# Kernel optimization log

Hardware: AMD Instinct MI355X
Metric: run time of the kernel (lower is better)

## Reference

```python
import jax, jax.numpy as jnp
import numpy as np

NUM_BLOCKS = 8
SPARSITY = 0.01
HARD_FRAC = 1.0
HSF = 1  # hidden_size_factor
SCALE = 0.02


def _softshrink(v, lambd):
    return jnp.where(v > lambd, v - lambd, jnp.where(v < -lambd, v + lambd, jnp.zeros_like(v)))


def setup_inputs() -> dict:
    key = jax.random.key(0)
    ks = jax.random.split(key, 5)
    B, H, W, C = 8, 128, 128, 768
    bs = C // NUM_BLOCKS  # 96
    x = jax.random.normal(ks[0], (B, H, W, C), dtype=jnp.float32)
    w1 = SCALE * jax.random.normal(ks[1], (2, NUM_BLOCKS, bs, bs * HSF), dtype=jnp.float32)
    b1 = SCALE * jax.random.normal(ks[2], (2, NUM_BLOCKS, bs * HSF), dtype=jnp.float32)
    w2 = SCALE * jax.random.normal(ks[3], (2, NUM_BLOCKS, bs * HSF, bs), dtype=jnp.float32)
    b2 = SCALE * jax.random.normal(ks[4], (2, NUM_BLOCKS, bs), dtype=jnp.float32)
    return {"x": x, "w1": w1, "b1": b1, "w2": w2, "b2": b2}


def reference(x, w1, b1, w2, b2):
    B, H, W, C = x.shape
    bs = C // NUM_BLOCKS
    bias = x
    xf = jnp.fft.rfft2(x, axes=(1, 2), norm="ortho")  # [B,H,W//2+1,C] complex
    Wf = W // 2 + 1
    xf = xf.reshape(B, H, Wf, NUM_BLOCKS, bs)
    total_modes = H // 2 + 1
    kept = int(total_modes * HARD_FRAC)
    h0 = total_modes - kept
    h1 = min(total_modes + kept, H)  # python slicing clips; mirror that statically
    w1k = min(kept, Wf)
    xs = xf[:, h0:h1, :w1k]  # kept-modes window
    xr, xi = jnp.real(xs), jnp.imag(xs)
    # block-diagonal complex MLP layer 1 with relu
    o1r = jax.nn.relu(jnp.einsum("bhwni,nio->bhwno", xr, w1[0]) - jnp.einsum("bhwni,nio->bhwno", xi, w1[1]) + b1[0])
    o1i = jax.nn.relu(jnp.einsum("bhwni,nio->bhwno", xi, w1[0]) + jnp.einsum("bhwni,nio->bhwno", xr, w1[1]) + b1[1])
    # layer 2
    o2r = jnp.einsum("bhwno,noi->bhwni", o1r, w2[0]) - jnp.einsum("bhwno,noi->bhwni", o1i, w2[1]) + b2[0]
    o2i = jnp.einsum("bhwno,noi->bhwni", o1i, w2[0]) + jnp.einsum("bhwno,noi->bhwni", o1r, w2[1]) + b2[1]
    # softshrink applied to real and imag components separately (torch stacks then shrinks)
    o2r = _softshrink(o2r, SPARSITY)
    o2i = _softshrink(o2i, SPARSITY)
    out = jnp.zeros((B, H, Wf, NUM_BLOCKS, bs), dtype=xf.dtype)
    out = out.at[:, h0:h1, :w1k].set(o2r + 1j * o2i)
    out = out.reshape(B, H, Wf, C)
    y = jnp.fft.irfft2(out, s=(H, W), axes=(1, 2), norm="ortho")
    return y + bias
```

## Files before the change

### kernel.cpp

```cpp
#include <hip/hip_runtime.h>


#define B_DIM 8
#define H_DIM 128
#define W_DIM 128
#define C_DIM 768
#define WF    65
#define NBLK  8
#define BS    96
#define LAMBDA 0.01f
#define TWO_PI_OVER_N 0.04908738521234052f

__device__ __forceinline__ int brev7(int v) { return (int)(__brev((unsigned)v) >> 25); }

__global__ __launch_bounds__(256) void k1_rfft_w(const float* __restrict__ x,
                                                 float2* __restrict__ S) {
    const int blk   = blockIdx.x;
    const int ctile = blk % 24;
    const int bh    = blk / 24;
    const int c0    = ctile * 32;

    __shared__ float2 zs[W_DIM][17];
    __shared__ float cs[64], sn[64];

    const int tid = threadIdx.x;
    if (tid < 64) {
        float sv, cv;
        sincosf(TWO_PI_OVER_N * (float)tid, &sv, &cv);
        cs[tid] = cv; sn[tid] = sv;
    }
    const float2* xp = (const float2*)(x + (size_t)bh * (W_DIM * C_DIM) + c0);
    for (int idx = tid; idx < W_DIM * 16; idx += 256) {
        int w = idx >> 4, u = idx & 15;
        zs[w][u] = xp[(size_t)w * (C_DIM / 2) + u];
    }
    __syncthreads();

    const int u  = tid & 15;
    const int j0 = tid >> 4;
    #pragma unroll
    for (int s = 0; s < 7; ++s) {
        const int ls = 6 - s;
        const int m  = 1 << ls;
        #pragma unroll
        for (int jj = 0; jj < 4; ++jj) {
            const int j  = j0 + jj * 16;
            const int t  = j & (m - 1);
            const int i0 = 2 * j - t;
            const int i1 = i0 + m;
            const int tw = t << (6 - ls);
            float2 a = zs[i0][u], b = zs[i1][u];
            const float cv = cs[tw], sv = sn[tw];
            float dx = a.x - b.x, dy = a.y - b.y;
            zs[i0][u] = make_float2(a.x + b.x, a.y + b.y);
            zs[i1][u] = make_float2(fmaf(dx, cv,  dy * sv),
                                    fmaf(dy, cv, -dx * sv));
        }
        __syncthreads();
    }

    for (int pos = tid; pos < WF * 16; pos += 256) {
        int kw = pos >> 4, uu = pos & 15;
        float2 Za = zs[brev7(kw)][uu];
        float2 Zb = zs[brev7((128 - kw) & 127)][uu];
        const float sc = 0.5f * 0.0078125f;
        float xcx = (Za.x + Zb.x) * sc;
        float xcy = (Za.y - Zb.y) * sc;
        float xdx = (Za.y + Zb.y) * sc;
        float xdy = (Zb.x - Za.x) * sc;
        float4* Srow = (float4*)(S + ((size_t)bh * WF + kw) * C_DIM + c0);
        Srow[uu] = make_float4(xcx, xcy, xdx, xdy);
    }
}

template <bool INV>
__global__ __launch_bounds__(256) void k_fft_h(float2* __restrict__ S) {
    const int blk   = blockIdx.x;
    const int ctile = blk % 24;
    const int rest  = blk / 24;
    const int kw    = rest % WF;
    const int b     = rest / WF;
    const int c0    = ctile * 32;

    __shared__ float2 zs[H_DIM][33];
    __shared__ float cs[64], sn[64];

    const int tid = threadIdx.x;
    if (tid < 64) {
        float sv, cv;
        sincosf(TWO_PI_OVER_N * (float)tid, &sv, &cv);
        cs[tid] = cv; sn[tid] = sv;
    }
    const size_t base = (((size_t)b * H_DIM) * WF + kw) * C_DIM + c0;
    const size_t hstr = (size_t)WF * C_DIM;
    for (int idx = tid; idx < H_DIM * 32; idx += 256) {
        int h = idx >> 5, c = idx & 31;
        zs[h][c] = S[base + (size_t)h * hstr + c];
    }
    __syncthreads();

    const int c  = tid & 31;
    const int j0 = tid >> 5;
    #pragma unroll
    for (int s = 0; s < 7; ++s) {
        const int ls = INV ? s : (6 - s);
        const int m  = 1 << ls;
        #pragma unroll
        for (int jj = 0; jj < 8; ++jj) {
            const int j  = j0 + jj * 8;
            const int t  = j & (m - 1);
            const int i0 = 2 * j - t;
            const int i1 = i0 + m;
            const int tw = t << (6 - ls);
            float2 a  = zs[i0][c];
            float2 bv = zs[i1][c];
            const float cv = cs[tw], sv = sn[tw];
            if (!INV) {
                float dx = a.x - bv.x, dy = a.y - bv.y;
                zs[i0][c] = make_float2(a.x + bv.x, a.y + bv.y);
                zs[i1][c] = make_float2(fmaf(dx, cv,  dy * sv),
                                        fmaf(dy, cv, -dx * sv));
            } else {
                float btx = fmaf(bv.x, cv, -bv.y * sv);
                float bty = fmaf(bv.y, cv,  bv.x * sv);
                zs[i0][c] = make_float2(a.x + btx, a.y + bty);
                zs[i1][c] = make_float2(a.x - btx, a.y - bty);
            }
        }
        __syncthreads();
    }

    for (int idx = tid; idx < H_DIM * 32; idx += 256) {
        int h = idx >> 5, cc = idx & 31;
        float2 v = zs[h][cc];
        if (INV) { v.x *= 0.0078125f; v.y *= 0.0078125f; }
        S[base + (size_t)h * hstr + cc] = v;
    }
}

__device__ __forceinline__ float softshrinkf(float v) {
    return v > LAMBDA ? v - LAMBDA : (v < -LAMBDA ? v + LAMBDA : 0.f);
}

__global__ __launch_bounds__(256) void k3_mlp(float2* __restrict__ S,
                                              const float* __restrict__ w1,
                                              const float* __restrict__ b1,
                                              const float* __restrict__ w2,
                                              const float* __restrict__ b2) {
    const int n     = blockIdx.y;
    const int pbase = blockIdx.x * 32;
    const int c0    = n * BS;

    __shared__ float2 xin[32][BS];
    __shared__ float2 o1s[32][BS];

    const int tid = threadIdx.x;
    for (int idx = tid; idx < 32 * BS; idx += 256) {
        int p = idx / BS, c = idx - p * BS;
        xin[p][c] = S[(size_t)(pbase + p) * C_DIM + c0 + c];
    }
    __syncthreads();

    const int oq = tid & 31;
    const int pq = tid >> 5;

    float ar[3][4], ai[3][4];
    #pragma unroll
    for (int k = 0; k < 3; ++k)
        #pragma unroll
        for (int jj = 0; jj < 4; ++jj) { ar[k][jj] = 0.f; ai[k][jj] = 0.f; }

    const float* W1r = w1 + (size_t)n * BS * BS + oq;
    const float* W1i = w1 + (size_t)(NBLK + n) * BS * BS + oq;
    for (int i = 0; i < BS; ++i) {
        float2 z0 = xin[pq][i];
        float2 z1 = xin[pq + 8][i];
        float2 z2 = xin[pq + 16][i];
        float2 z3 = xin[pq + 24][i];
        #pragma unroll
        for (int k = 0; k < 3; ++k) {
            float wr = W1r[i * BS + 32 * k];
            float wi = W1i[i * BS + 32 * k];
            ar[k][0] = fmaf(z0.x, wr, fmaf(-z0.y, wi, ar[k][0]));
            ai[k][0] = fmaf(z0.y, wr, fmaf( z0.x, wi, ai[k][0]));
            ar[k][1] = fmaf(z1.x, wr, fmaf(-z1.y, wi, ar[k][1]));
            ai[k][1] = fmaf(z1.y, wr, fmaf( z1.x, wi, ai[k][1]));
            ar[k][2] = fmaf(z2.x, wr, fmaf(-z2.y, wi, ar[k][2]));
            ai[k][2] = fmaf(z2.y, wr, fmaf( z2.x, wi, ai[k][2]));
            ar[k][3] = fmaf(z3.x, wr, fmaf(-z3.y, wi, ar[k][3]));
            ai[k][3] = fmaf(z3.y, wr, fmaf( z3.x, wi, ai[k][3]));
        }
    }
    #pragma unroll
    for (int k = 0; k < 3; ++k) {
        const int o = oq + 32 * k;
        const float br = b1[n * BS + o], bi = b1[(NBLK + n) * BS + o];
        #pragma unroll
        for (int jj = 0; jj < 4; ++jj)
            o1s[pq + 8 * jj][o] = make_float2(fmaxf(ar[k][jj] + br, 0.f),
                                              fmaxf(ai[k][jj] + bi, 0.f));
    }
    __syncthreads();

    #pragma unroll
    for (int k = 0; k < 3; ++k)
        #pragma unroll
        for (int jj = 0; jj < 4; ++jj) { ar[k][jj] = 0.f; ai[k][jj] = 0.f; }

    const float* W2r = w2 + (size_t)n * BS * BS + oq;
    const float* W2i = w2 + (size_t)(NBLK + n) * BS * BS + oq;
    for (int i = 0; i < BS; ++i) {
        float2 z0 = o1s[pq][i];
        float2 z1 = o1s[pq + 8][i];
        float2 z2 = o1s[pq + 16][i];
        float2 z3 = o1s[pq + 24][i];
        #pragma unroll
        for (int k = 0; k < 3; ++k) {
            float wr = W2r[i * BS + 32 * k];
            float wi = W2i[i * BS + 32 * k];
            ar[k][0] = fmaf(z0.x, wr, fmaf(-z0.y, wi, ar[k][0]));
            ai[k][0] = fmaf(z0.y, wr, fmaf( z0.x, wi, ai[k][0]));
            ar[k][1] = fmaf(z1.x, wr, fmaf(-z1.y, wi, ar[k][1]));
            ai[k][1] = fmaf(z1.y, wr, fmaf( z1.x, wi, ai[k][1]));
            ar[k][2] = fmaf(z2.x, wr, fmaf(-z2.y, wi, ar[k][2]));
            ai[k][2] = fmaf(z2.y, wr, fmaf( z2.x, wi, ai[k][2]));
            ar[k][3] = fmaf(z3.x, wr, fmaf(-z3.y, wi, ar[k][3]));
            ai[k][3] = fmaf(z3.y, wr, fmaf( z3.x, wi, ai[k][3]));
        }
    }
    #pragma unroll
    for (int k = 0; k < 3; ++k) {
        const int o = oq + 32 * k;
        const float br = b2[n * BS + o], bi = b2[(NBLK + n) * BS + o];
        #pragma unroll
        for (int jj = 0; jj < 4; ++jj) {
            float vr = softshrinkf(ar[k][jj] + br);
            float vi = softshrinkf(ai[k][jj] + bi);
            S[(size_t)(pbase + pq + 8 * jj) * C_DIM + c0 + o] = make_float2(vr, vi);
        }
    }
}

__global__ __launch_bounds__(256) void k5_irfft_w(const float2* __restrict__ S,
                                                  const float* __restrict__ x,
                                                  float* __restrict__ out) {
    const int blk   = blockIdx.x;
    const int ctile = blk % 24;
    const int bh    = blk / 24;
    const int c0    = ctile * 32;

    __shared__ float2 zs[W_DIM][17];
    __shared__ float cs[64], sn[64];

    const int tid = threadIdx.x;
    if (tid < 64) {
        float sv, cv;
        sincosf(TWO_PI_OVER_N * (float)tid, &sv, &cv);
        cs[tid] = cv; sn[tid] = sv;
    }
    for (int pos = tid; pos < WF * 16; pos += 256) {
        int kw = pos >> 4, uu = pos & 15;
        float4 q = ((const float4*)(S + ((size_t)bh * WF + kw) * C_DIM + c0))[uu];
        float xcx = q.x, xcy = q.y, xdx = q.z, xdy = q.w;
        if (kw == 0 || kw == 64) { xcy = 0.f; xdy = 0.f; }
        zs[kw][uu] = make_float2(xcx - xdy, xcy + xdx);
        if (kw >= 1 && kw <= 63)
            zs[128 - kw][uu] = make_float2(xcx + xdy, xdx - xcy);
    }
    __syncthreads();

    const int u  = tid & 15;
    const int j0 = tid >> 4;
    #pragma unroll
    for (int s = 0; s < 7; ++s) {
        const int ls = 6 - s;
        const int m  = 1 << ls;
        #pragma unroll
        for (int jj = 0; jj < 4; ++jj) {
            const int j  = j0 + jj * 16;
            const int t  = j & (m - 1);
            const int i0 = 2 * j - t;
            const int i1 = i0 + m;
            const int tw = t << (6 - ls);
            float2 a = zs[i0][u], b = zs[i1][u];
            const float cv = cs[tw], sv = sn[tw];
            float dx = a.x - b.x, dy = a.y - b.y;
            zs[i0][u] = make_float2(a.x + b.x, a.y + b.y);
            zs[i1][u] = make_float2(fmaf(dx, cv, -dy * sv),
                                    fmaf(dy, cv,  dx * sv));
        }
        __syncthreads();
    }

    const size_t obase = (size_t)bh * (W_DIM * C_DIM) + c0;
    for (int pos = tid; pos < W_DIM * 16; pos += 256) {
        int p = pos >> 4, uu = pos & 15;
        int w = brev7(p);
        float2 v  = zs[p][uu];
        float2 xv = ((const float2*)(x + obase + (size_t)w * C_DIM))[uu];
        ((float2*)(out + obase + (size_t)w * C_DIM))[uu] =
            make_float2(v.x + xv.x, v.y + xv.y);
    }
}

extern "C" void kernel_launch(void* const* d_in, const int* in_sizes, int n_in,
                              void* d_out, int out_size, void* d_ws, size_t ws_size,
                              hipStream_t stream) {
    const float* x  = (const float*)d_in[0];
    const float* w1 = (const float*)d_in[1];
    const float* b1 = (const float*)d_in[2];
    const float* w2 = (const float*)d_in[3];
    const float* b2 = (const float*)d_in[4];
    float* out = (float*)d_out;
    float2* S  = (float2*)d_ws;

    k1_rfft_w<<<dim3(B_DIM * H_DIM * 24), dim3(256), 0, stream>>>(x, S);
    k_fft_h<false><<<dim3(B_DIM * WF * 24), dim3(256), 0, stream>>>(S);
    k3_mlp<<<dim3((B_DIM * H_DIM * WF) / 32, NBLK), dim3(256), 0, stream>>>(S, w1, b1, w2, b2);
    k_fft_h<true><<<dim3(B_DIM * WF * 24), dim3(256), 0, stream>>>(S);
    k5_irfft_w<<<dim3(B_DIM * H_DIM * 24), dim3(256), 0, stream>>>(S, x, out);
}
```

Measured before the change: 2.526 ms.

## Run spectral block MLP on bf16 MFMA with hi/lo split precision

```diff
diff --git a/kernel.cpp b/kernel.cpp
--- a/kernel.cpp
+++ b/kernel.cpp
@@ -11,7 +11,42 @@
 #define LAMBDA 0.01f
 #define TWO_PI_OVER_N 0.04908738521234052f
 
+typedef short bf16x8 __attribute__((ext_vector_type(8)));
+typedef float f32x4  __attribute__((ext_vector_type(4)));
+
 __device__ __forceinline__ int brev7(int v) { return (int)(__brev((unsigned)v) >> 25); }
+
+__device__ __forceinline__ void split_bf16(float f, short& h, short& l) {
+    unsigned u  = __float_as_uint(f);
+    unsigned hr = u + 0x7FFFu + ((u >> 16) & 1u);
+    h = (short)(hr >> 16);
+    float hf = __uint_as_float((hr >> 16) << 16);
+    float lo = f - hf;
+    unsigned u2 = __float_as_uint(lo);
+    unsigned lr = u2 + 0x7FFFu + ((u2 >> 16) & 1u);
+    l = (short)(lr >> 16);
+}
+
+__global__ __launch_bounds__(256) void k0_wconv(const float* __restrict__ w1,
+                                                const float* __restrict__ w2,
+                                                short* __restrict__ bt) {
+    int idx = blockIdx.x * 256 + threadIdx.x;
+    int k   = idx % 192;
+    int col = (idx / 192) % 96;
+    int v   = (idx / (192 * 96)) % 2;
+    int n   = (idx / (192 * 96 * 2)) % 8;
+    int L   = idx / (192 * 96 * 2 * 8);
+    const float* W  = L ? w2 : w1;
+    const float* Wr = W + (size_t)n * 9216;
+    const float* Wi = W + (size_t)(8 + n) * 9216;
+    float val;
+    if (v == 0) val = (k < 96) ? Wr[k * 96 + col] : -Wi[(k - 96) * 96 + col];
+    else        val = (k < 96) ? Wi[k * 96 + col] :  Wr[(k - 96) * 96 + col];
+    short h, l; split_bf16(val, h, l);
+    size_t mi = ((size_t)(L * 8 + n) * 2 + v) * 2;
+    bt[(mi + 0) * 18432 + col * 192 + k] = h;
+    bt[(mi + 1) * 18432 + col * 192 + k] = l;
+}
 
 __global__ __launch_bounds__(256) void k1_rfft_w(const float* __restrict__ x,
                                                  float2* __restrict__ S) {
@@ -142,102 +177,140 @@
     return v > LAMBDA ? v - LAMBDA : (v < -LAMBDA ? v + LAMBDA : 0.f);
 }
 
-__global__ __launch_bounds__(256) void k3_mlp(float2* __restrict__ S,
-                                              const float* __restrict__ w1,
-                                              const float* __restrict__ b1,
-                                              const float* __restrict__ w2,
-                                              const float* __restrict__ b2) {
+__global__ __launch_bounds__(512, 2) void k3_mfma(float2* __restrict__ S,
+                                                  const short* __restrict__ bt,
+                                                  const float* __restrict__ b1,
+                                                  const float* __restrict__ b2) {
     const int n     = blockIdx.y;
-    const int pbase = blockIdx.x * 32;
+    const int pbase = blockIdx.x * 128;
     const int c0    = n * BS;
 
-    __shared__ float2 xin[32][BS];
-    __shared__ float2 o1s[32][BS];
-
-    const int tid = threadIdx.x;
-    for (int idx = tid; idx < 32 * BS; idx += 256) {
-        int p = idx / BS, c = idx - p * BS;
-        xin[p][c] = S[(size_t)(pbase + p) * C_DIM + c0 + c];
-    }
-    __syncthreads();
-
-    const int oq = tid & 31;
-    const int pq = tid >> 5;
-
-    float ar[3][4], ai[3][4];
-    #pragma unroll
-    for (int k = 0; k < 3; ++k)
-        #pragma unroll
-        for (int jj = 0; jj < 4; ++jj) { ar[k][jj] = 0.f; ai[k][jj] = 0.f; }
-
-    const float* W1r = w1 + (size_t)n * BS * BS + oq;
-    const float* W1i = w1 + (size_t)(NBLK + n) * BS * BS + oq;
-    for (int i = 0; i < BS; ++i) {
-        float2 z0 = xin[pq][i];
-        float2 z1 = xin[pq + 8][i];
-        float2 z2 = xin[pq + 16][i];
-        float2 z3 = xin[pq + 24][i];
-        #pragma unroll
-        for (int k = 0; k < 3; ++k) {
-            float wr = W1r[i * BS + 32 * k];
-            float wi = W1i[i * BS + 32 * k];
-            ar[k][0] = fmaf(z0.x, wr, fmaf(-z0.y, wi, ar[k][0]));
-            ai[k][0] = fmaf(z0.y, wr, fmaf( z0.x, wi, ai[k][0]));
-            ar[k][1] = fmaf(z1.x, wr, fmaf(-z1.y, wi, ar[k][1]));
-            ai[k][1] = fmaf(z1.y, wr, fmaf( z1.x, wi, ai[k][1]));
-            ar[k][2] = fmaf(z2.x, wr, fmaf(-z2.y, wi, ar[k][2]));
-            ai[k][2] = fmaf(z2.y, wr, fmaf( z2.x, wi, ai[k][2]));
-            ar[k][3] = fmaf(z3.x, wr, fmaf(-z3.y, wi, ar[k][3]));
-            ai[k][3] = fmaf(z3.y, wr, fmaf( z3.x, wi, ai[k][3]));
-        }
-    }
-    #pragma unroll
-    for (int k = 0; k < 3; ++k) {
-        const int o = oq + 32 * k;
-        const float br = b1[n * BS + o], bi = b1[(NBLK + n) * BS + o];
-        #pragma unroll
-        for (int jj = 0; jj < 4; ++jj)
-            o1s[pq + 8 * jj][o] = make_float2(fmaxf(ar[k][jj] + br, 0.f),
-                                              fmaxf(ai[k][jj] + bi, 0.f));
-    }
-    __syncthreads();
-
-    #pragma unroll
-    for (int k = 0; k < 3; ++k)
-        #pragma unroll
-        for (int jj = 0; jj < 4; ++jj) { ar[k][jj] = 0.f; ai[k][jj] = 0.f; }
-
-    const float* W2r = w2 + (size_t)n * BS * BS + oq;
-    const float* W2i = w2 + (size_t)(NBLK + n) * BS * BS + oq;
-    for (int i = 0; i < BS; ++i) {
-        float2 z0 = o1s[pq][i];
-        float2 z1 = o1s[pq + 8][i];
-        float2 z2 = o1s[pq + 16][i];
-        float2 z3 = o1s[pq + 24][i];
-        #pragma unroll
-        for (int k = 0; k < 3; ++k) {
-            float wr = W2r[i * BS + 32 * k];
-            float wi = W2i[i * BS + 32 * k];
-            ar[k][0] = fmaf(z0.x, wr, fmaf(-z0.y, wi, ar[k][0]));
-            ai[k][0] = fmaf(z0.y, wr, fmaf( z0.x, wi, ai[k][0]));
-            ar[k][1] = fmaf(z1.x, wr, fmaf(-z1.y, wi, ar[k][1]));
-            ai[k][1] = fmaf(z1.y, wr, fmaf( z1.x, wi, ai[k][1]));
-            ar[k][2] = fmaf(z2.x, wr, fmaf(-z2.y, wi, ar[k][2]));
-            ai[k][2] = fmaf(z2.y, wr, fmaf( z2.x, wi, ai[k][2]));
-            ar[k][3] = fmaf(z3.x, wr, fmaf(-z3.y, wi, ar[k][3]));
-            ai[k][3] = fmaf(z3.y, wr, fmaf( z3.x, wi, ai[k][3]));
-        }
-    }
-    #pragma unroll
-    for (int k = 0; k < 3; ++k) {
-        const int o = oq + 32 * k;
-        const float br = b2[n * BS + o], bi = b2[(NBLK + n) * BS + o];
-        #pragma unroll
-        for (int jj = 0; jj < 4; ++jj) {
-            float vr = softshrinkf(ar[k][jj] + br);
-            float vi = softshrinkf(ai[k][jj] + bi);
-            S[(size_t)(pbase + pq + 8 * jj) * C_DIM + c0 + o] = make_float2(vr, vi);
-        }
+    __shared__ short Ah[128][200];
+    __shared__ short Al[128][200];
+
+    const int tid  = threadIdx.x;
+    const int lane = tid & 63;
+    const int wv   = tid >> 6;
+    const int wm   = wv >> 1;
+    const int wn   = wv & 1;
+    const int l15  = lane & 15;
+    const int lk8  = (lane >> 4) * 8;
+    const int lr4  = (lane >> 4) * 4;
+
+    for (int idx = tid; idx < 128 * 96; idx += 512) {
+        int m = idx / 96, c = idx - m * 96;
+        float2 z = S[(size_t)(pbase + m) * C_DIM + c0 + c];
+        short h, l;
+        split_bf16(z.x, h, l); Ah[m][c]      = h; Al[m][c]      = l;
+        split_bf16(z.y, h, l); Ah[m][96 + c] = h; Al[m][96 + c] = l;
+    }
+    __syncthreads();
+
+    const short* bt1h = bt + ((size_t)((0 * 8 + n) * 2 + wn) * 2 + 0) * 18432;
+    const short* bt1l = bt1h + 18432;
+    const short* bt2h = bt + ((size_t)((1 * 8 + n) * 2 + wn) * 2 + 0) * 18432;
+    const short* bt2l = bt2h + 18432;
+
+    f32x4 acc[2][6];
+    #pragma unroll
+    for (int ma = 0; ma < 2; ++ma)
+        #pragma unroll
+        for (int nb = 0; nb < 6; ++nb) acc[ma][nb] = (f32x4){0.f, 0.f, 0.f, 0.f};
+
+    for (int ks = 0; ks < 6; ++ks) {
+        const int koff = ks * 32 + lk8;
+        bf16x8 ah[2], al[2];
+        #pragma unroll
+        for (int ma = 0; ma < 2; ++ma) {
+            const int row = wm * 32 + ma * 16 + l15;
+            ah[ma] = *(const bf16x8*)&Ah[row][koff];
+            al[ma] = *(const bf16x8*)&Al[row][koff];
+        }
+        bf16x8 bh[6], bl[6];
+        #pragma unroll
+        for (int nb = 0; nb < 6; ++nb) {
+            const int cl = nb * 16 + l15;
+            bh[nb] = *(const bf16x8*)(bt1h + cl * 192 + koff);
+            bl[nb] = *(const bf16x8*)(bt1l + cl * 192 + koff);
+        }
+        #pragma unroll
+        for (int ma = 0; ma < 2; ++ma)
+            #pragma unroll
+            for (int nb = 0; nb < 6; ++nb) {
+                acc[ma][nb] = __builtin_amdgcn_mfma_f32_16x16x32_bf16(ah[ma], bh[nb], acc[ma][nb], 0, 0, 0);
+                acc[ma][nb] = __builtin_amdgcn_mfma_f32_16x16x32_bf16(ah[ma], bl[nb], acc[ma][nb], 0, 0, 0);
+                acc[ma][nb] = __builtin_amdgcn_mfma_f32_16x16x32_bf16(al[ma], bh[nb], acc[ma][nb], 0, 0, 0);
+            }
+    }
+    __syncthreads();
+
+    {
+        const float* b1p = b1 + (size_t)(wn * 8 + n) * 96;
+        #pragma unroll
+        for (int ma = 0; ma < 2; ++ma)
+            #pragma unroll
+            for (int nb = 0; nb < 6; ++nb) {
+                const int cl = nb * 16 + l15;
+                const float bb = b1p[cl];
+                const int kdst = wn * 96 + cl;
+                #pragma unroll
+                for (int j = 0; j < 4; ++j) {
+                    const int row = wm * 32 + ma * 16 + lr4 + j;
+                    float v = fmaxf(acc[ma][nb][j] + bb, 0.f);
+                    short h, l; split_bf16(v, h, l);
+                    Ah[row][kdst] = h; Al[row][kdst] = l;
+                }
+            }
+    }
+    __syncthreads();
+
+    #pragma unroll
+    for (int ma = 0; ma < 2; ++ma)
+        #pragma unroll
+        for (int nb = 0; nb < 6; ++nb) acc[ma][nb] = (f32x4){0.f, 0.f, 0.f, 0.f};
+
+    for (int ks = 0; ks < 6; ++ks) {
+        const int koff = ks * 32 + lk8;
+        bf16x8 ah[2], al[2];
+        #pragma unroll
+        for (int ma = 0; ma < 2; ++ma) {
+            const int row = wm * 32 + ma * 16 + l15;
+            ah[ma] = *(const bf16x8*)&Ah[row][koff];
+            al[ma] = *(const bf16x8*)&Al[row][koff];
+        }
+        bf16x8 bh[6], bl[6];
+        #pragma unroll
+        for (int nb = 0; nb < 6; ++nb) {
+            const int cl = nb * 16 + l15;
+            bh[nb] = *(const bf16x8*)(bt2h + cl * 192 + koff);
+            bl[nb] = *(const bf16x8*)(bt2l + cl * 192 + koff);
+        }
+        #pragma unroll
+        for (int ma = 0; ma < 2; ++ma)
+            #pragma unroll
+            for (int nb = 0; nb < 6; ++nb) {
+                acc[ma][nb] = __builtin_amdgcn_mfma_f32_16x16x32_bf16(ah[ma], bh[nb], acc[ma][nb], 0, 0, 0);
+                acc[ma][nb] = __builtin_amdgcn_mfma_f32_16x16x32_bf16(ah[ma], bl[nb], acc[ma][nb], 0, 0, 0);
+                acc[ma][nb] = __builtin_amdgcn_mfma_f32_16x16x32_bf16(al[ma], bh[nb], acc[ma][nb], 0, 0, 0);
+            }
+    }
+
+    {
+        const float* b2p = b2 + (size_t)(wn * 8 + n) * 96;
+        #pragma unroll
+        for (int ma = 0; ma < 2; ++ma)
+            #pragma unroll
+            for (int nb = 0; nb < 6; ++nb) {
+                const int cl = nb * 16 + l15;
+                const float bb = b2p[cl];
+                #pragma unroll
+                for (int j = 0; j < 4; ++j) {
+                    const int row = wm * 32 + ma * 16 + lr4 + j;
+                    float v = softshrinkf(acc[ma][nb][j] + bb);
+                    float* dst = (float*)(S + (size_t)(pbase + row) * C_DIM + c0 + cl) + wn;
+                    *dst = v;
+                }
+            }
     }
 }
 
@@ -313,10 +386,12 @@
     const float* b2 = (const float*)d_in[4];
     float* out = (float*)d_out;
     float2* S  = (float2*)d_ws;
-
+    short* bt  = (short*)d_out;
+
+    k0_wconv<<<dim3(2304), dim3(256), 0, stream>>>(w1, w2, bt);
     k1_rfft_w<<<dim3(B_DIM * H_DIM * 24), dim3(256), 0, stream>>>(x, S);
     k_fft_h<false><<<dim3(B_DIM * WF * 24), dim3(256), 0, stream>>>(S);
-    k3_mlp<<<dim3((B_DIM * H_DIM * WF) / 32, NBLK), dim3(256), 0, stream>>>(S, w1, b1, w2, b2);
+    k3_mfma<<<dim3((B_DIM * H_DIM * WF) / 128, NBLK), dim3(512), 0, stream>>>(S, bt, b1, b2);
     k_fft_h<true><<<dim3(B_DIM * WF * 24), dim3(256), 0, stream>>>(S);
     k5_irfft_w<<<dim3(B_DIM * H_DIM * 24), dim3(256), 0, stream>>>(S, x, out);
 }
```

Measured after the change: 2.291 ms. 9.3% less time.
